# Kernel optimization log

Hardware: AMD Instinct MI355X
Metric: run time of the kernel (lower is better)

The kernel has to match this reference:

```python
import jax, jax.numpy as jnp
import numpy as np

B, S, D = 4, 2048, 16
N_HEAD_ARG = 16
# Faithful to source bug: effective num heads = hidden_size (D), head_size = D // n_head_arg.
# This only type-checks when head_size == 1 (D == n_head_arg), as in the repo config.
HEADS = D                     # self.n_head = hidden_size
HEAD_SIZE = D // N_HEAD_ARG   # = 1


def setup_inputs() -> dict:
    key = jax.random.key(0)
    k_x, k_wq, k_bq, k_wo, k_bo = jax.random.split(key, 5)
    x = jax.random.normal(k_x, (B, S, D), dtype=jnp.float32)
    # torch Linear init scale ~ 1/sqrt(in_features); store weights as [in, out]
    s = 1.0 / np.sqrt(D)
    w_qkv = jax.random.uniform(k_wq, (D, 3 * D), minval=-s, maxval=s, dtype=jnp.float32)
    b_qkv = jax.random.uniform(k_bq, (3 * D,), minval=-s, maxval=s, dtype=jnp.float32)
    w_out = jax.random.uniform(k_wo, (D, D), minval=-s, maxval=s, dtype=jnp.float32)
    b_out = jax.random.uniform(k_bo, (D,), minval=-s, maxval=s, dtype=jnp.float32)
    return {"x": x, "w_qkv": w_qkv, "b_qkv": b_qkv, "w_out": w_out, "b_out": b_out}


def reference(x, w_qkv, b_qkv, w_out, b_out):
    b, s, _ = x.shape
    qkv = x @ w_qkv + b_qkv                      # [b, s, 3D]
    q, k, v = jnp.split(qkv, 3, axis=-1)         # each [b, s, D]
    # [b, s, H, hs] -> [b, H, s, hs]
    q = q.reshape(b, s, HEADS, HEAD_SIZE).transpose(0, 2, 1, 3)
    k = k.reshape(b, s, HEADS, HEAD_SIZE).transpose(0, 2, 1, 3)
    v = v.reshape(b, s, HEADS, HEAD_SIZE).transpose(0, 2, 1, 3)
    scale = 1.0 / jnp.sqrt(jnp.asarray(HEAD_SIZE, dtype=x.dtype))
    scores = jnp.einsum('bhqd,bhkd->bhqk', q, k) * scale   # [b, H, s, s]
    causal = jnp.tril(jnp.ones((s, s), dtype=bool))
    scores = jnp.where(causal, scores, jnp.asarray(-jnp.inf, dtype=scores.dtype))
    attn = jax.nn.softmax(scores, axis=-1)
    # dropout is identity in eval mode (correctness baseline)
    out = jnp.einsum('bhqk,bhkd->bhqd', attn, v)            # [b, H, s, hs]
    out = out.transpose(0, 2, 1, 3).reshape(b, s, HEADS * HEAD_SIZE)
    return out @ w_out + b_out
```

## Files before the change

kernel.cpp:

```cpp
#include <hip/hip_runtime.h>
#include <math.h>

#define BB 4
#define SS 2048
#define DD 16
#define HH 16
#define NM 32

#define EXP2(x) __builtin_amdgcn_exp2f(x)
#define LOG2E 1.44269504088896340736f

__constant__ float INVFACT[NM] = {
    1.000000000e+00f, 1.000000000e+00f, 5.000000000e-01f, 1.666666667e-01f,
    4.166666667e-02f, 8.333333333e-03f, 1.388888889e-03f, 1.984126984e-04f,
    2.480158730e-05f, 2.755731922e-06f, 2.755731922e-07f, 2.505210839e-08f,
    2.087675699e-09f, 1.605904384e-10f, 1.147074560e-11f, 7.647163732e-13f,
    4.779477332e-14f, 2.811457254e-15f, 1.561920697e-16f, 8.220635247e-18f,
    4.110317623e-19f, 1.957294106e-20f, 8.896791392e-22f, 3.868170171e-23f,
    1.611737571e-24f, 6.446950284e-26f, 2.479596263e-27f, 9.183689864e-29f,
    3.279889237e-30f, 1.130996289e-31f, 3.769987629e-33f, 1.216125042e-34f};

#define UNPACK16(X4, XR)                                                \
  const float4 x0_ = (X4)[0], x1_ = (X4)[1], x2_ = (X4)[2], x3_ = (X4)[3]; \
  const float XR[16] = {x0_.x, x0_.y, x0_.z, x0_.w, x1_.x, x1_.y, x1_.z, \
                        x1_.w, x2_.x, x2_.y, x2_.z, x2_.w, x3_.x, x3_.y, \
                        x3_.z, x3_.w};

__global__ __launch_bounds__(256) void moment_kernel(
    const float* __restrict__ x, const float* __restrict__ w_qkv,
    const float* __restrict__ b_qkv, float* __restrict__ MT) {
  __shared__ float kl[512];
  __shared__ float vl[512];
  const int blk = blockIdx.x;
  const int sub = blk & 3;
  const int bh = blk >> 2;
  const int b = bh >> 4, h = bh & 15;
  const int t = threadIdx.x;

  float wk[16], wv[16];
#pragma unroll
  for (int i = 0; i < 16; ++i) {
    wk[i] = w_qkv[i * 48 + 16 + h];
    wv[i] = w_qkv[i * 48 + 32 + h];
  }
  const float bk = b_qkv[16 + h], bv = b_qkv[32 + h];

#pragma unroll
  for (int rr = 0; rr < 2; ++rr) {
    const int jl = rr * 256 + t;
    const int j = sub * 512 + jl;
    const float4* X4 = (const float4*)(x + ((size_t)b * SS + j) * DD);
    UNPACK16(X4, xr);
    float k = bk, v = bv;
#pragma unroll
    for (int i = 0; i < 16; ++i) {
      k = fmaf(xr[i], wk[i], k);
      v = fmaf(xr[i], wv[i], v);
    }
    kl[jl] = k;
    vl[jl] = v;
  }
  __syncthreads();

  const int m = t & 31;
  const int jl = t >> 5;
  const int jb = sub * 8 + jl;
  float s = 0.f, tv = 0.f;
  const int base = jl * 64;
  for (int u = 0; u < 64; ++u) {
    const float k = kl[base + u];
    const float v = vl[base + u];
    const float k2 = k * k, k4 = k2 * k2, k8 = k4 * k4, k16 = k8 * k8;
    float p = (m & 1) ? k : 1.f;
    p *= (m & 2) ? k2 : 1.f;
    p *= (m & 4) ? k4 : 1.f;
    p *= (m & 8) ? k8 : 1.f;
    p *= (m & 16) ? k16 : 1.f;
    s += p;
    tv = fmaf(p, v, tv);
  }
  float* row = MT + ((size_t)bh * 32 + jb) * 64;
  row[m] = s;
  row[32 + m] = tv;
}

__global__ __launch_bounds__(64) void attn_kernel(
    const float* __restrict__ x, const float* __restrict__ w_qkv,
    const float* __restrict__ b_qkv, const float* __restrict__ MT,
    float* __restrict__ AO) {
  __shared__ float kd[64], vd[64], bc[64];
  const int blk = blockIdx.x;
  const int qb = blk & 31;
  const int bh = blk >> 5;
  const int b = bh >> 4, h = bh & 15;
  const int lane = threadIdx.x;

  float wq[16], wk[16], wv[16];
#pragma unroll
  for (int i = 0; i < 16; ++i) {
    wq[i] = w_qkv[i * 48 + h];
    wk[i] = w_qkv[i * 48 + 16 + h];
    wv[i] = w_qkv[i * 48 + 32 + h];
  }

  const int i0 = qb * 64 + lane;
  const float4* X4 = (const float4*)(x + ((size_t)b * SS + i0) * DD);
  UNPACK16(X4, xr);
  float q = b_qkv[h], k = b_qkv[16 + h], v = b_qkv[32 + h];
#pragma unroll
  for (int i = 0; i < 16; ++i) {
    q = fmaf(xr[i], wq[i], q);
    k = fmaf(xr[i], wk[i], k);
    v = fmaf(xr[i], wv[i], v);
  }
  kd[lane] = k;
  vd[lane] = v;
  const float qs = q * LOG2E;

  if (qb > 0) {
    const float* mtb = MT + (size_t)bh * 32 * 64 + lane;
    float acc = 0.f;
    for (int jb = 0; jb < qb; ++jb) acc += mtb[jb * 64];
    const float c = INVFACT[lane & 31];
    const int slot = (lane < 32) ? (2 * lane) : (2 * (lane - 32) + 1);
    bc[slot] = acc * c;
  }
  __syncthreads();

  float num = 0.f, den = 0.f;
  if (qb > 0) {
    const float2* bc2 = (const float2*)bc;
    float p = 1.f;
#pragma unroll
    for (int m = 0; m < NM; ++m) {
      const float2 st = bc2[m];
      den = fmaf(p, st.x, den);
      num = fmaf(p, st.y, num);
      p *= q;
    }
  }

  float ld = 0.f, ad = 0.f;
  const float4* kd4 = (const float4*)kd;
  const float4* vd4 = (const float4*)vd;
#pragma unroll
  for (int g = 0; g < 16; ++g) {
    const float4 k4 = kd4[g], v4 = vd4[g];
    const int jj = 4 * g;
    float e;
    e = EXP2(qs * k4.x); e = (jj + 0 <= lane) ? e : 0.f; ld += e; ad = fmaf(e, v4.x, ad);
    e = EXP2(qs * k4.y); e = (jj + 1 <= lane) ? e : 0.f; ld += e; ad = fmaf(e, v4.y, ad);
    e = EXP2(qs * k4.z); e = (jj + 2 <= lane) ? e : 0.f; ld += e; ad = fmaf(e, v4.z, ad);
    e = EXP2(qs * k4.w); e = (jj + 3 <= lane) ? e : 0.f; ld += e; ad = fmaf(e, v4.w, ad);
  }

  AO[(size_t)bh * SS + i0] = (ad + num) / (ld + den);
}

__global__ __launch_bounds__(256) void proj_kernel(
    const float* __restrict__ AO, const float* __restrict__ w,
    const float* __restrict__ bias, float* __restrict__ out) {
  __shared__ float wct[DD * 68];
  __shared__ float aol[256];
  __shared__ float bs[DD];
  const int t = threadIdx.x;
  const int b = blockIdx.x >> 7;
  const int s_base = (blockIdx.x * 16) & (SS - 1);

  wct[(t & 15) * 68 + (t >> 4)] = w[t];
  if (t < DD) bs[t] = bias[t];
  {
    const int h = t >> 4, row_l = t & 15;
    const int bh = b * HH + h;
    aol[row_l * 16 + h] = AO[(size_t)bh * SS + s_base + row_l];
  }
  __syncthreads();

  const int row_l = t >> 4, d = t & 15;
  const float4* ao4 = (const float4*)aol;
  const float4* wc4 = (const float4*)wct;

  float y = bs[d];
#pragma unroll
  for (int g = 0; g < 4; ++g) {
    const float4 xv = ao4[row_l * 4 + g];
    const float4 wv = wc4[d * 17 + g];
    y = fmaf(xv.x, wv.x, y);
    y = fmaf(xv.y, wv.y, y);
    y = fmaf(xv.z, wv.z, y);
    y = fmaf(xv.w, wv.w, y);
  }
  out[(size_t)blockIdx.x * 256 + t] = y;
}

extern "C" void kernel_launch(void* const* d_in, const int* in_sizes, int n_in,
                              void* d_out, int out_size, void* d_ws,
                              size_t ws_size, hipStream_t stream) {
  const float* x = (const float*)d_in[0];
  const float* w_qkv = (const float*)d_in[1];
  const float* b_qkv = (const float*)d_in[2];
  const float* w_out = (const float*)d_in[3];
  const float* b_out = (const float*)d_in[4];
  float* out = (float*)d_out;

  float* ws = (float*)d_ws;
  float* MT = ws;
  float* AO = ws + 64 * 32 * 64;

  moment_kernel<<<256, 256, 0, stream>>>(x, w_qkv, b_qkv, MT);
  attn_kernel<<<2048, 64, 0, stream>>>(x, w_qkv, b_qkv, MT, AO);
  proj_kernel<<<512, 256, 0, stream>>>(AO, w_out, b_out, out);
}
```

Baseline: 80.61 us.

## Fuse attention and output projection into one kernel, fold factorial scaling into moments

```diff
diff --git a/kernel.cpp b/kernel.cpp
--- a/kernel.cpp
+++ b/kernel.cpp
@@ -20,10 +20,10 @@
     1.611737571e-24f, 6.446950284e-26f, 2.479596263e-27f, 9.183689864e-29f,
     3.279889237e-30f, 1.130996289e-31f, 3.769987629e-33f, 1.216125042e-34f};
 
-#define UNPACK16(X4, XR)                                                \
+#define UNPACK16(X4, XR)                                                   \
   const float4 x0_ = (X4)[0], x1_ = (X4)[1], x2_ = (X4)[2], x3_ = (X4)[3]; \
-  const float XR[16] = {x0_.x, x0_.y, x0_.z, x0_.w, x1_.x, x1_.y, x1_.z, \
-                        x1_.w, x2_.x, x2_.y, x2_.z, x2_.w, x3_.x, x3_.y, \
+  const float XR[16] = {x0_.x, x0_.y, x0_.z, x0_.w, x1_.x, x1_.y, x1_.z,   \
+                        x1_.w, x2_.x, x2_.y, x2_.z, x2_.w, x3_.x, x3_.y,   \
                         x3_.z, x3_.w};
 
 __global__ __launch_bounds__(256) void moment_kernel(
@@ -79,118 +79,111 @@
     s += p;
     tv = fmaf(p, v, tv);
   }
+  const float c = INVFACT[m];
   float* row = MT + ((size_t)bh * 32 + jb) * 64;
-  row[m] = s;
-  row[32 + m] = tv;
+  row[m] = s * c;
+  row[32 + m] = tv * c;
 }
 
-__global__ __launch_bounds__(64) void attn_kernel(
+__global__ __launch_bounds__(256) void attn_proj_kernel(
     const float* __restrict__ x, const float* __restrict__ w_qkv,
     const float* __restrict__ b_qkv, const float* __restrict__ MT,
-    float* __restrict__ AO) {
-  __shared__ float kd[64], vd[64], bc[64];
+    const float* __restrict__ w_out, const float* __restrict__ b_out,
+    float* __restrict__ out) {
+  __shared__ float wct[DD * 68];
+  __shared__ float bso[DD];
+  __shared__ float bc[4][64];
+  __shared__ float kd[4][64];
+  __shared__ float vd[4][64];
+  __shared__ float aol[64 * 16];
   const int blk = blockIdx.x;
   const int qb = blk & 31;
-  const int bh = blk >> 5;
-  const int b = bh >> 4, h = bh & 15;
-  const int lane = threadIdx.x;
-
-  float wq[16], wk[16], wv[16];
-#pragma unroll
-  for (int i = 0; i < 16; ++i) {
-    wq[i] = w_qkv[i * 48 + h];
-    wk[i] = w_qkv[i * 48 + 16 + h];
-    wv[i] = w_qkv[i * 48 + 32 + h];
-  }
+  const int b = blk >> 5;
+  const int t = threadIdx.x;
+  const int w = __builtin_amdgcn_readfirstlane(t >> 6);
+  const int lane = t & 63;
+
+  wct[(t & 15) * 68 + (t >> 4)] = w_out[t];
+  if (t < DD) bso[t] = b_out[t];
 
   const int i0 = qb * 64 + lane;
   const float4* X4 = (const float4*)(x + ((size_t)b * SS + i0) * DD);
   UNPACK16(X4, xr);
-  float q = b_qkv[h], k = b_qkv[16 + h], v = b_qkv[32 + h];
-#pragma unroll
-  for (int i = 0; i < 16; ++i) {
-    q = fmaf(xr[i], wq[i], q);
-    k = fmaf(xr[i], wk[i], k);
-    v = fmaf(xr[i], wv[i], v);
-  }
-  kd[lane] = k;
-  vd[lane] = v;
-  const float qs = q * LOG2E;
-
-  if (qb > 0) {
-    const float* mtb = MT + (size_t)bh * 32 * 64 + lane;
-    float acc = 0.f;
-    for (int jb = 0; jb < qb; ++jb) acc += mtb[jb * 64];
-    const float c = INVFACT[lane & 31];
-    const int slot = (lane < 32) ? (2 * lane) : (2 * (lane - 32) + 1);
-    bc[slot] = acc * c;
-  }
-  __syncthreads();
-
-  float num = 0.f, den = 0.f;
-  if (qb > 0) {
-    const float2* bc2 = (const float2*)bc;
-    float p = 1.f;
-#pragma unroll
-    for (int m = 0; m < NM; ++m) {
-      const float2 st = bc2[m];
-      den = fmaf(p, st.x, den);
-      num = fmaf(p, st.y, num);
-      p *= q;
-    }
-  }
-
-  float ld = 0.f, ad = 0.f;
-  const float4* kd4 = (const float4*)kd;
-  const float4* vd4 = (const float4*)vd;
-#pragma unroll
-  for (int g = 0; g < 16; ++g) {
-    const float4 k4 = kd4[g], v4 = vd4[g];
-    const int jj = 4 * g;
-    float e;
-    e = EXP2(qs * k4.x); e = (jj + 0 <= lane) ? e : 0.f; ld += e; ad = fmaf(e, v4.x, ad);
-    e = EXP2(qs * k4.y); e = (jj + 1 <= lane) ? e : 0.f; ld += e; ad = fmaf(e, v4.y, ad);
-    e = EXP2(qs * k4.z); e = (jj + 2 <= lane) ? e : 0.f; ld += e; ad = fmaf(e, v4.z, ad);
-    e = EXP2(qs * k4.w); e = (jj + 3 <= lane) ? e : 0.f; ld += e; ad = fmaf(e, v4.w, ad);
-  }
-
-  AO[(size_t)bh * SS + i0] = (ad + num) / (ld + den);
-}
-
-__global__ __launch_bounds__(256) void proj_kernel(
-    const float* __restrict__ AO, const float* __restrict__ w,
-    const float* __restrict__ bias, float* __restrict__ out) {
-  __shared__ float wct[DD * 68];
-  __shared__ float aol[256];
-  __shared__ float bs[DD];
-  const int t = threadIdx.x;
-  const int b = blockIdx.x >> 7;
-  const int s_base = (blockIdx.x * 16) & (SS - 1);
-
-  wct[(t & 15) * 68 + (t >> 4)] = w[t];
-  if (t < DD) bs[t] = bias[t];
-  {
-    const int h = t >> 4, row_l = t & 15;
+
+#pragma unroll
+  for (int hh = 0; hh < 4; ++hh) {
+    const int h = w * 4 + hh;
     const int bh = b * HH + h;
-    aol[row_l * 16 + h] = AO[(size_t)bh * SS + s_base + row_l];
-  }
-  __syncthreads();
-
-  const int row_l = t >> 4, d = t & 15;
-  const float4* ao4 = (const float4*)aol;
-  const float4* wc4 = (const float4*)wct;
-
-  float y = bs[d];
-#pragma unroll
-  for (int g = 0; g < 4; ++g) {
-    const float4 xv = ao4[row_l * 4 + g];
-    const float4 wv = wc4[d * 17 + g];
-    y = fmaf(xv.x, wv.x, y);
-    y = fmaf(xv.y, wv.y, y);
-    y = fmaf(xv.z, wv.z, y);
-    y = fmaf(xv.w, wv.w, y);
-  }
-  out[(size_t)blockIdx.x * 256 + t] = y;
+
+    float q = b_qkv[h], k = b_qkv[16 + h], v = b_qkv[32 + h];
+#pragma unroll
+    for (int i = 0; i < 16; ++i) {
+      q = fmaf(xr[i], w_qkv[i * 48 + h], q);
+      k = fmaf(xr[i], w_qkv[i * 48 + 16 + h], k);
+      v = fmaf(xr[i], w_qkv[i * 48 + 32 + h], v);
+    }
+    kd[w][lane] = k;
+    vd[w][lane] = v;
+
+    if (qb > 0) {
+      const float* mtb = MT + (size_t)bh * 32 * 64 + lane;
+      float acc = 0.f;
+      for (int jb = 0; jb < qb; ++jb) acc += mtb[jb * 64];
+      const int slot = (lane < 32) ? (2 * lane) : (2 * (lane - 32) + 1);
+      bc[w][slot] = acc;
+    }
+    __syncthreads();
+
+    float num = 0.f, den = 0.f;
+    if (qb > 0) {
+      const float2* bc2 = (const float2*)bc[w];
+      float p = 1.f;
+#pragma unroll
+      for (int m = 0; m < NM; ++m) {
+        const float2 st = bc2[m];
+        den = fmaf(p, st.x, den);
+        num = fmaf(p, st.y, num);
+        p *= q;
+      }
+    }
+
+    const float qs = q * LOG2E;
+    float ld = 0.f, ad = 0.f;
+    const float4* kd4 = (const float4*)kd[w];
+    const float4* vd4 = (const float4*)vd[w];
+#pragma unroll
+    for (int g = 0; g < 16; ++g) {
+      const float4 k4 = kd4[g], v4 = vd4[g];
+      const int jj = 4 * g;
+      float e;
+      e = EXP2(qs * k4.x); e = (jj + 0 <= lane) ? e : 0.f; ld += e; ad = fmaf(e, v4.x, ad);
+      e = EXP2(qs * k4.y); e = (jj + 1 <= lane) ? e : 0.f; ld += e; ad = fmaf(e, v4.y, ad);
+      e = EXP2(qs * k4.z); e = (jj + 2 <= lane) ? e : 0.f; ld += e; ad = fmaf(e, v4.z, ad);
+      e = EXP2(qs * k4.w); e = (jj + 3 <= lane) ? e : 0.f; ld += e; ad = fmaf(e, v4.w, ad);
+    }
+
+    aol[lane * 16 + h] = (ad + num) / (ld + den);
+    __syncthreads();
+  }
+
+#pragma unroll
+  for (int rep = 0; rep < 4; ++rep) {
+    const int e = rep * 256 + t;
+    const int row_l = e >> 4, d = e & 15;
+    const float4* ao4 = (const float4*)(aol + row_l * 16);
+    const float4* wc4 = (const float4*)(wct + d * 68);
+    float y = bso[d];
+#pragma unroll
+    for (int g = 0; g < 4; ++g) {
+      const float4 xv = ao4[g];
+      const float4 wv = wc4[g];
+      y = fmaf(xv.x, wv.x, y);
+      y = fmaf(xv.y, wv.y, y);
+      y = fmaf(xv.z, wv.z, y);
+      y = fmaf(xv.w, wv.w, y);
+    }
+    out[((size_t)b * SS + qb * 64) * DD + e] = y;
+  }
 }
 
 extern "C" void kernel_launch(void* const* d_in, const int* in_sizes, int n_in,
@@ -203,11 +196,9 @@
   const float* b_out = (const float*)d_in[4];
   float* out = (float*)d_out;
 
-  float* ws = (float*)d_ws;
-  float* MT = ws;
-  float* AO = ws + 64 * 32 * 64;
+  float* MT = (float*)d_ws;
 
   moment_kernel<<<256, 256, 0, stream>>>(x, w_qkv, b_qkv, MT);
-  attn_kernel<<<2048, 64, 0, stream>>>(x, w_qkv, b_qkv, MT, AO);
-  proj_kernel<<<512, 256, 0, stream>>>(AO, w_out, b_out, out);
+  attn_proj_kernel<<<128, 256, 0, stream>>>(x, w_qkv, b_qkv, MT, w_out,
+                                            b_out, out);
 }
```

Measured after the change: 95.60 us. 1.19x slower.
